# Kernel optimization log

Hardware: AMD Instinct MI355X
Metric: run time of the kernel (lower is better)

The kernel has to match this reference:

```python
import jax, jax.numpy as jnp
import numpy as np

NUM_HEADS = 16


def setup_inputs() -> dict:
    key = jax.random.key(0)
    k1, k2, k3 = jax.random.split(key, 3)
    T, B, E = 2048, 2, 1024
    query = jax.random.normal(k1, (T, B, E), dtype=jnp.float32)
    # xavier-uniform-ish init for qkv weight, small normal for output proj
    lim = (6.0 / (3 * E + E)) ** 0.5
    W_qkv = jax.random.uniform(k2, (3 * E, E), dtype=jnp.float32, minval=-lim, maxval=lim)
    W_o = jax.random.normal(k3, (E, E), dtype=jnp.float32) * 0.02
    b_qkv = jnp.zeros((3 * E,), dtype=jnp.float32)
    b_o = jnp.zeros((E,), dtype=jnp.float32)
    return {"query": query, "W_qkv": W_qkv, "b_qkv": b_qkv, "W_o": W_o, "b_o": b_o}


def reference(query, W_qkv, b_qkv, W_o, b_o):
    T, B, E = query.shape
    H = NUM_HEADS
    hd = E // H
    scaling = float(hd) ** -0.5

    # fused qkv projection: [T, B, 3E]
    qkv = jnp.einsum('tbe,fe->tbf', query, W_qkv) + b_qkv
    q, k, v = jnp.split(qkv, 3, axis=-1)
    q = q * scaling

    def to_heads(x):  # [T, B, E] -> [B*H, T, hd]
        return x.reshape(T, B * H, hd).transpose(1, 0, 2)

    q, k, v = to_heads(q), to_heads(k), to_heads(v)

    # explicit bmm QK^T -> softmax -> bmm AV (faithful to source)
    scores = jnp.einsum('bqd,bkd->bqk', q, k)          # [B*H, T, T]
    attn = jax.nn.softmax(scores, axis=-1)             # dropout p=0.0 (eval)
    ctx = jnp.einsum('bqk,bkd->bqd', attn, v)          # [B*H, T, hd]

    out = ctx.transpose(1, 0, 2).reshape(T, B, E)
    out = jnp.einsum('tbe,fe->tbf', out, W_o) + b_o    # o_net

    avg_weights = attn.reshape(B, H, T, T).sum(axis=1) / H  # need_weights=True path
    return out, avg_weights
```

## Files before the change

kernel.cpp:

```cpp
#include <hip/hip_runtime.h>
#include <stdint.h>

typedef unsigned short u16;
typedef __bf16 bf16x8 __attribute__((ext_vector_type(8)));
typedef float f32x4 __attribute__((ext_vector_type(4)));
typedef float f32x16 __attribute__((ext_vector_type(16)));

__device__ __forceinline__ u16 f2b(float f) {
  unsigned u = __builtin_bit_cast(unsigned, f);
  u += 0x7fffu + ((u >> 16) & 1u);
  return (u16)(u >> 16);
}

__device__ __forceinline__ float fexp2(float x) { return __builtin_amdgcn_exp2f(x); }

__device__ __forceinline__ void gld_lds16(const void* g, void* l) {
  __builtin_amdgcn_global_load_lds((const __attribute__((address_space(1))) unsigned int*)g,
                                   (__attribute__((address_space(3))) unsigned int*)l,
                                   16, 0, 0);
}

__global__ __launch_bounds__(256) void k_cvt(const float* __restrict__ s,
                                             u16* __restrict__ d, int n4) {
  int i = blockIdx.x * 256 + threadIdx.x;
  if (i >= n4) return;
  float4 v = reinterpret_cast<const float4*>(s)[i];
  ushort4 o;
  o.x = f2b(v.x); o.y = f2b(v.y); o.z = f2b(v.z); o.w = f2b(v.w);
  reinterpret_cast<ushort4*>(d)[i] = o;
}

template <int EPI>
__global__ __launch_bounds__(256) void k_gemm_nt(
    const u16* __restrict__ A, const u16* __restrict__ B, const float* __restrict__ bias,
    float* __restrict__ outF, u16* __restrict__ q_ws, u16* __restrict__ k_ws,
    u16* __restrict__ vt_ws) {
  __shared__ u16 Al[2][4096];
  __shared__ u16 Bl[2][4096];
  const int tid = threadIdx.x;
  const int w = tid >> 6, lane = tid & 63;
  const int wr = w >> 1, wc = w & 1;
  const int lo = lane & 15, hi = lane >> 4;
  const int tm = blockIdx.y, tn = blockIdx.x;
  const size_t arow0 = (size_t)tm * 128;
  const size_t brow0 = (size_t)tn * 128;

  f32x4 acc[4][4] = {};

  const int rr = lane >> 2;
  const int kc = (lane & 3) * 8;

  {
    const int k0 = kc;
    for (int rs = 0; rs < 2; ++rs) {
      int seg = rs * 4 + w;
      gld_lds16(A + (arow0 + seg * 16 + rr) * 1024 + k0, &Al[0][seg * 512 + lane * 8]);
      gld_lds16(B + (brow0 + seg * 16 + rr) * 1024 + k0, &Bl[0][seg * 512 + lane * 8]);
    }
  }
  __syncthreads();
  int cur = 0;
  for (int kb = 0; kb < 32; ++kb) {
    if (kb + 1 < 32) {
      const int k0 = (kb + 1) * 32 + kc;
      for (int rs = 0; rs < 2; ++rs) {
        int seg = rs * 4 + w;
        gld_lds16(A + (arow0 + seg * 16 + rr) * 1024 + k0, &Al[cur ^ 1][seg * 512 + lane * 8]);
        gld_lds16(B + (brow0 + seg * 16 + rr) * 1024 + k0, &Bl[cur ^ 1][seg * 512 + lane * 8]);
      }
    }
    bf16x8 af[4], bfr[4];
#pragma unroll
    for (int m = 0; m < 4; ++m)
      af[m] = *(const bf16x8*)&Al[cur][(wr * 64 + m * 16 + lo) * 32 + hi * 8];
#pragma unroll
    for (int n = 0; n < 4; ++n)
      bfr[n] = *(const bf16x8*)&Bl[cur][(wc * 64 + n * 16 + lo) * 32 + hi * 8];
#pragma unroll
    for (int m = 0; m < 4; ++m)
#pragma unroll
      for (int n = 0; n < 4; ++n)
        acc[m][n] = __builtin_amdgcn_mfma_f32_16x16x32_bf16(af[m], bfr[n], acc[m][n], 0, 0, 0);
    __syncthreads();
    cur ^= 1;
  }

  if (EPI == 0) {
#pragma unroll
    for (int n = 0; n < 4; ++n) {
      const int col = tn * 128 + wc * 64 + n * 16 + lo;
      const float bb = bias[col];
#pragma unroll
      for (int m = 0; m < 4; ++m)
#pragma unroll
        for (int r = 0; r < 4; ++r) {
          const int row = tm * 128 + wr * 64 + m * 16 + hi * 4 + r;
          outF[(size_t)row * 1024 + col] = acc[m][n][r] + bb;
        }
    }
  } else {
    const int sec = tn >> 3;
#pragma unroll
    for (int n = 0; n < 4; ++n) {
      const int cin = (tn & 7) * 128 + wc * 64 + n * 16 + lo;
      const int h = cin >> 6, d = cin & 63;
      const float bb = bias[sec * 1024 + cin];
#pragma unroll
      for (int m = 0; m < 4; ++m) {
        const int rowb = tm * 128 + wr * 64 + m * 16 + hi * 4;
        const int t0 = rowb >> 1;
        const float v0 = acc[m][n][0] + bb, v1 = acc[m][n][1] + bb;
        const float v2 = acc[m][n][2] + bb, v3 = acc[m][n][3] + bb;
        if (sec == 0) {
          const float s = 0.18033688f;
          q_ws[(((size_t)h * 2048 + t0) * 64) + d]            = f2b(v0 * s);
          q_ws[(((size_t)(16 + h) * 2048 + t0) * 64) + d]     = f2b(v1 * s);
          q_ws[(((size_t)h * 2048 + t0 + 1) * 64) + d]        = f2b(v2 * s);
          q_ws[(((size_t)(16 + h) * 2048 + t0 + 1) * 64) + d] = f2b(v3 * s);
        } else if (sec == 1) {
          k_ws[(((size_t)h * 2048 + t0) * 64) + d]            = f2b(v0);
          k_ws[(((size_t)(16 + h) * 2048 + t0) * 64) + d]     = f2b(v1);
          k_ws[(((size_t)h * 2048 + t0 + 1) * 64) + d]        = f2b(v2);
          k_ws[(((size_t)(16 + h) * 2048 + t0 + 1) * 64) + d] = f2b(v3);
        } else {
          const int tp0 = (t0 & ~12) | ((t0 & 4) << 1) | ((t0 & 8) >> 1);
          ushort2 p0, p1;
          p0.x = f2b(v0); p0.y = f2b(v2);
          p1.x = f2b(v1); p1.y = f2b(v3);
          *(ushort2*)(vt_ws + ((size_t)h * 64 + d) * 2048 + tp0) = p0;
          *(ushort2*)(vt_ws + ((size_t)(16 + h) * 64 + d) * 2048 + tp0) = p1;
        }
      }
    }
  }
}

__global__ __launch_bounds__(512) void k_flash(
    const u16* __restrict__ q_ws, const u16* __restrict__ k_ws, const u16* __restrict__ vt_ws,
    u16* __restrict__ ctx_ws, float* __restrict__ c_ws) {
  __shared__ __align__(16) u16 KVl[32768];
  const int tid = threadIdx.x, w = tid >> 6, lane = tid & 63;
  const int h = lane >> 5, l31 = lane & 31, l7 = lane & 7;
  const int hh = w >> 2;
  const int wq = w & 3;
  const int tid_h = tid & 255;

  const int flat = blockIdx.y * 16 + blockIdx.x;
  const int xcd = flat & 7, slot = flat >> 3;
  const int bh = xcd * 4 + (slot >> 4);
  const int qtile = slot & 15;
  const int b = bh >> 4, head = bh & 15;
  const int qbase = qtile * 128;
  const int qrow = qbase + wq * 32 + l31;

  bf16x8 qf[4];
#pragma unroll
  for (int j = 0; j < 4; ++j)
    qf[j] = *(const bf16x8*)(q_ws + ((size_t)bh * 2048 + qrow) * 64 + j * 16 + h * 8);

  const int srow = tid_h >> 3, schk = tid_h & 7;
  const int xc = (schk ^ (srow & 7)) * 8;
  const u16* kgA = k_ws + ((size_t)bh * 2048 + hh * 16 * 64 + srow) * 64 + xc;
  const u16* vgA = vt_ws + ((size_t)bh * 64 + srow) * 2048 + hh * 16 * 64 + xc;

  f32x16 ca0 = {}, ca1 = {};
  float lrow = 0.f;

  {
    u16* base = KVl + hh * 8192;
    gld_lds16(kgA,             base + tid_h * 8);
    gld_lds16(kgA + 32 * 64,   base + 2048 + tid_h * 8);
    gld_lds16(vgA,             base + 4096 + tid_h * 8);
    gld_lds16(vgA + 32 * 2048, base + 6144 + tid_h * 8);
  }
  __syncthreads();

  int cur = 0;
  for (int it = 0; it < 16; ++it) {
    if (it < 15) {
      u16* base = KVl + (cur ^ 1) * 16384 + hh * 8192;
      const u16* kgt = kgA + (size_t)(it + 1) * 4096;
      const u16* vgt = vgA + (it + 1) * 64;
      gld_lds16(kgt,             base + tid_h * 8);
      gld_lds16(kgt + 32 * 64,   base + 2048 + tid_h * 8);
      gld_lds16(vgt,             base + 4096 + tid_h * 8);
      gld_lds16(vgt + 32 * 2048, base + 6144 + tid_h * 8);
    }
    const char* Kb = (const char*)(KVl + cur * 16384 + hh * 8192);
    const char* Vb = Kb + 8192;

    f32x16 st0 = {}, st1 = {};
    __builtin_amdgcn_s_setprio(1);
#pragma unroll
    for (int j = 0; j < 4; ++j) {
      bf16x8 k0 = *(const bf16x8*)(Kb + l31 * 128 + (((2 * j + h) ^ l7) * 16));
      bf16x8 k1 = *(const bf16x8*)(Kb + (32 + l31) * 128 + (((2 * j + h) ^ l7) * 16));
      st0 = __builtin_amdgcn_mfma_f32_32x32x16_bf16(k0, qf[j], st0, 0, 0, 0);
      st1 = __builtin_amdgcn_mfma_f32_32x32x16_bf16(k1, qf[j], st1, 0, 0, 0);
    }
    __builtin_amdgcn_s_setprio(0);

    float ps0 = 0.f, ps1 = 0.f;
#pragma unroll
    for (int r = 0; r < 16; ++r) { float p = fexp2(st0[r]); st0[r] = p; ps0 += p; }
#pragma unroll
    for (int r = 0; r < 16; ++r) { float p = fexp2(st1[r]); st1[r] = p; ps1 += p; }
    float ps = ps0 + ps1;
    ps += __shfl_xor(ps, 32, 64);
    lrow += ps;

    bf16x8 pb00, pb01, pb10, pb11;
#pragma unroll
    for (int i = 0; i < 8; ++i) {
      pb00[i] = (__bf16)st0[i];
      pb01[i] = (__bf16)st0[8 + i];
      pb10[i] = (__bf16)st1[i];
      pb11[i] = (__bf16)st1[8 + i];
    }

    __builtin_amdgcn_s_setprio(1);
#pragma unroll
    for (int t2 = 0; t2 < 2; ++t2)
#pragma unroll
      for (int kp = 0; kp < 2; ++kp) {
        const int ch = (4 * t2 + 2 * kp + h) ^ l7;
        bf16x8 v0 = *(const bf16x8*)(Vb + l31 * 128 + ch * 16);
        bf16x8 v1 = *(const bf16x8*)(Vb + (32 + l31) * 128 + ch * 16);
        const bf16x8 pv = (t2 == 0) ? (kp == 0 ? pb00 : pb01) : (kp == 0 ? pb10 : pb11);
        ca0 = __builtin_amdgcn_mfma_f32_32x32x16_bf16(v0, pv, ca0, 0, 0, 0);
        ca1 = __builtin_amdgcn_mfma_f32_32x32x16_bf16(v1, pv, ca1, 0, 0, 0);
      }
    __builtin_amdgcn_s_setprio(0);

    __syncthreads();
    cur ^= 1;
  }

  float* F = (float*)KVl;
  if (w >= 4) {
    const int g = w - 4;
#pragma unroll
    for (int r = 0; r < 16; ++r) {
      F[g * 2048 + r * 64 + lane] = ca0[r];
      F[g * 2048 + (16 + r) * 64 + lane] = ca1[r];
    }
    F[8192 + g * 64 + lane] = lrow;
  }
  __syncthreads();
  u16* tw = (u16*)((char*)KVl + 34816 + w * 4096);
  if (w < 4) {
#pragma unroll
    for (int r = 0; r < 16; ++r) {
      ca0[r] += F[w * 2048 + r * 64 + lane];
      ca1[r] += F[w * 2048 + (16 + r) * 64 + lane];
    }
    lrow += F[8192 + w * 64 + lane];
    const float inv = 1.0f / lrow;
    if (lane < 32) c_ws[(size_t)bh * 2048 + qrow] = inv;
#pragma unroll
    for (int r = 0; r < 16; ++r) {
      const int d0 = (r & 3) + 8 * (r >> 2) + 4 * h;
      const int d1 = 32 + d0;
      *(u16*)((char*)tw + l31 * 128 + ((2 * d0) ^ (l7 << 4))) = f2b(ca0[r] * inv);
      *(u16*)((char*)tw + l31 * 128 + ((2 * d1) ^ (l7 << 4))) = f2b(ca1[r] * inv);
    }
  }
  __syncthreads();
  if (w < 4) {
#pragma unroll
    for (int it = 0; it < 4; ++it) {
      const int row = it * 8 + (lane >> 3);
      uint4 val = *(const uint4*)((const char*)tw + row * 128 + (((lane & 7) ^ (row & 7)) * 16));
      const int q = qbase + wq * 32 + row;
      *(uint4*)(ctx_ws + ((size_t)(q * 2 + b)) * 1024 + head * 64 + (lane & 7) * 8) = val;
    }
  }
}

__global__ __launch_bounds__(256) void k_avg(
    const u16* __restrict__ q_ws, const u16* __restrict__ k_ws,
    const float* __restrict__ c_ws, float* __restrict__ avg) {
  __shared__ __align__(16) u16 Kl[2][128 * 64];
  const int tid = threadIdx.x, w = tid >> 6, lane = tid & 63;
  const int lo = lane & 15, hi = lane >> 4;
  const int kbase = blockIdx.x * 128;
  const int qb = blockIdx.y * 64;
  const int b = blockIdx.z;
  const int qrow = qb + w * 16 + lo;
  const int qrow_base = qb + w * 16 + hi * 4;

  const int r0 = tid >> 3, c0 = tid & 7;
  const int ldsoff = r0 * 128 + ((c0 ^ (r0 & 7)) << 4);
  const u16* kg = k_ws + ((size_t)(b * 16) * 2048 + kbase + r0) * 64 + c0 * 8;
  const int l7 = lo & 7;

  float acc[8][4] = {};
  const f32x4 zero = {0.f, 0.f, 0.f, 0.f};

  uint4 rg0 = *(const uint4*)(kg);
  uint4 rg1 = *(const uint4*)(kg + 32 * 64);
  uint4 rg2 = *(const uint4*)(kg + 64 * 64);
  uint4 rg3 = *(const uint4*)(kg + 96 * 64);
  {
    char* dst = (char*)Kl[0] + ldsoff;
    *(uint4*)(dst) = rg0;
    *(uint4*)(dst + 32 * 128) = rg1;
    *(uint4*)(dst + 64 * 128) = rg2;
    *(uint4*)(dst + 96 * 128) = rg3;
  }
  __syncthreads();

  int cur = 0;
  for (int h = 0; h < 16; ++h) {
    const int bh = b * 16 + h;
    if (h + 1 < 16) {
      const u16* kgn = kg + (size_t)(h + 1) * 2048 * 64;
      rg0 = *(const uint4*)(kgn);
      rg1 = *(const uint4*)(kgn + 32 * 64);
      rg2 = *(const uint4*)(kgn + 64 * 64);
      rg3 = *(const uint4*)(kgn + 96 * 64);
    }
    const u16* qp = q_ws + ((size_t)bh * 2048 + qrow) * 64 + hi * 8;
    bf16x8 qf0 = *(const bf16x8*)qp;
    bf16x8 qf1 = *(const bf16x8*)(qp + 32);
    const float4 cf = *(const float4*)(c_ws + (size_t)bh * 2048 + qrow_base);
    const float cfa[4] = {cf.x, cf.y, cf.z, cf.w};
    const char* kbse = (const char*)Kl[cur];
#pragma unroll
    for (int n = 0; n < 8; ++n) {
      const char* kp = kbse + (n * 16 + lo) * 128;
      bf16x8 k0 = *(const bf16x8*)(kp + ((hi ^ l7) << 4));
      bf16x8 k1 = *(const bf16x8*)(kp + (((hi + 4) ^ l7) << 4));
      f32x4 s = __builtin_amdgcn_mfma_f32_16x16x32_bf16(qf0, k0, zero, 0, 0, 0);
      s = __builtin_amdgcn_mfma_f32_16x16x32_bf16(qf1, k1, s, 0, 0, 0);
#pragma unroll
      for (int r = 0; r < 4; ++r) acc[n][r] += fexp2(s[r]) * cfa[r];
    }
    if (h + 1 < 16) {
      char* dst = (char*)Kl[cur ^ 1] + ldsoff;
      *(uint4*)(dst) = rg0;
      *(uint4*)(dst + 32 * 128) = rg1;
      *(uint4*)(dst + 64 * 128) = rg2;
      *(uint4*)(dst + 96 * 128) = rg3;
      __syncthreads();
    }
    cur ^= 1;
  }

  const float s16 = 1.0f / 16.0f;
#pragma unroll
  for (int n = 0; n < 8; ++n)
#pragma unroll
    for (int r = 0; r < 4; ++r)
      avg[((size_t)(b * 2048 + qrow_base + r)) * 2048 + kbase + n * 16 + lo] = acc[n][r] * s16;
}

extern "C" void kernel_launch(void* const* d_in, const int* in_sizes, int n_in,
                              void* d_out, int out_size, void* d_ws, size_t ws_size,
                              hipStream_t stream) {
  const float* query = (const float*)d_in[0];
  const float* Wqkv  = (const float*)d_in[1];
  const float* bqkv  = (const float*)d_in[2];
  const float* Wo    = (const float*)d_in[3];
  const float* bo    = (const float*)d_in[4];
  float* out = (float*)d_out;
  float* avg = out + (size_t)4096 * 1024;

  char* ws = (char*)d_ws;
  u16* qbf    = (u16*)(ws);
  u16* ctx_ws = (u16*)(ws);
  u16*   wqkvbf = (u16*)(ws + 8388608);
  float* c_ws   = (float*)(ws + 8388608);
  u16* wobf  = (u16*)(ws + 14680064);
  u16* q_ws  = (u16*)(ws + 16777216);
  u16* k_ws  = (u16*)(ws + 25165824);
  u16* vt_ws = (u16*)(ws + 33554432);

  k_cvt<<<dim3(4096), dim3(256), 0, stream>>>(query, qbf, 1048576);
  k_cvt<<<dim3(3072), dim3(256), 0, stream>>>(Wqkv, wqkvbf, 786432);
  k_cvt<<<dim3(1024), dim3(256), 0, stream>>>(Wo, wobf, 262144);
  k_gemm_nt<1><<<dim3(24, 32), dim3(256), 0, stream>>>(
      qbf, wqkvbf, bqkv, nullptr, q_ws, k_ws, vt_ws);
  k_flash<<<dim3(16, 32), dim3(512), 0, stream>>>(
      q_ws, k_ws, vt_ws, ctx_ws, c_ws);
  k_avg<<<dim3(16, 32, 2), dim3(256), 0, stream>>>(
      q_ws, k_ws, c_ws, avg);
  k_gemm_nt<0><<<dim3(8, 32), dim3(256), 0, stream>>>(
      ctx_ws, wobf, bo, out, nullptr, nullptr, nullptr);
}
```

Baseline: 157.4 us.

## Double GEMM K-tile to 64 with XOR-swizzled LDS layout

The bf16 NT GEMM now stages 64-wide K tiles instead of 32-wide ones. That halves the number of main-loop iterations and barriers, with each tile feeding two MFMA sub-steps. The LDS layout uses an XOR swizzle of 16-byte chunks by row, so the fragment reads across lanes avoid bank conflicts. The barrier now sits at the top of each iteration, before the prefetch. This doubles the LDS footprint per block, which can reduce occupancy.

```diff
diff --git a/kernel.cpp b/kernel.cpp
--- a/kernel.cpp
+++ b/kernel.cpp
@@ -35,53 +35,61 @@
     const u16* __restrict__ A, const u16* __restrict__ B, const float* __restrict__ bias,
     float* __restrict__ outF, u16* __restrict__ q_ws, u16* __restrict__ k_ws,
     u16* __restrict__ vt_ws) {
-  __shared__ u16 Al[2][4096];
-  __shared__ u16 Bl[2][4096];
+  __shared__ __align__(16) u16 Al[2][8192];
+  __shared__ __align__(16) u16 Bl[2][8192];
   const int tid = threadIdx.x;
   const int w = tid >> 6, lane = tid & 63;
   const int wr = w >> 1, wc = w & 1;
   const int lo = lane & 15, hi = lane >> 4;
+  const int l7 = lane & 7;
   const int tm = blockIdx.y, tn = blockIdx.x;
   const size_t arow0 = (size_t)tm * 128;
   const size_t brow0 = (size_t)tn * 128;
 
   f32x4 acc[4][4] = {};
 
-  const int rr = lane >> 2;
-  const int kc = (lane & 3) * 8;
-
-  {
-    const int k0 = kc;
-    for (int rs = 0; rs < 2; ++rs) {
-      int seg = rs * 4 + w;
-      gld_lds16(A + (arow0 + seg * 16 + rr) * 1024 + k0, &Al[0][seg * 512 + lane * 8]);
-      gld_lds16(B + (brow0 + seg * 16 + rr) * 1024 + k0, &Bl[0][seg * 512 + lane * 8]);
-    }
-  }
-  __syncthreads();
+  const int rr0 = tid >> 3, cc = tid & 7;
+  const int xoff = (cc ^ (rr0 & 7)) * 8;
+  const u16* Asrc = A + (arow0 + rr0) * 1024 + xoff;
+  const u16* Bsrc = B + (brow0 + rr0) * 1024 + xoff;
+  const int ldst = rr0 * 64 + cc * 8;
+
+#pragma unroll
+  for (int j = 0; j < 4; ++j) {
+    gld_lds16(Asrc + j * 32 * 1024, &Al[0][ldst + j * 2048]);
+    gld_lds16(Bsrc + j * 32 * 1024, &Bl[0][ldst + j * 2048]);
+  }
+
   int cur = 0;
-  for (int kb = 0; kb < 32; ++kb) {
-    if (kb + 1 < 32) {
-      const int k0 = (kb + 1) * 32 + kc;
-      for (int rs = 0; rs < 2; ++rs) {
-        int seg = rs * 4 + w;
-        gld_lds16(A + (arow0 + seg * 16 + rr) * 1024 + k0, &Al[cur ^ 1][seg * 512 + lane * 8]);
-        gld_lds16(B + (brow0 + seg * 16 + rr) * 1024 + k0, &Bl[cur ^ 1][seg * 512 + lane * 8]);
-      }
-    }
-    bf16x8 af[4], bfr[4];
-#pragma unroll
-    for (int m = 0; m < 4; ++m)
-      af[m] = *(const bf16x8*)&Al[cur][(wr * 64 + m * 16 + lo) * 32 + hi * 8];
-#pragma unroll
-    for (int n = 0; n < 4; ++n)
-      bfr[n] = *(const bf16x8*)&Bl[cur][(wc * 64 + n * 16 + lo) * 32 + hi * 8];
-#pragma unroll
-    for (int m = 0; m < 4; ++m)
-#pragma unroll
-      for (int n = 0; n < 4; ++n)
-        acc[m][n] = __builtin_amdgcn_mfma_f32_16x16x32_bf16(af[m], bfr[n], acc[m][n], 0, 0, 0);
+  for (int kt = 0; kt < 16; ++kt) {
     __syncthreads();
+    if (kt < 15) {
+      const int koff = (kt + 1) * 64;
+#pragma unroll
+      for (int j = 0; j < 4; ++j) {
+        gld_lds16(Asrc + koff + j * 32 * 1024, &Al[cur ^ 1][ldst + j * 2048]);
+        gld_lds16(Bsrc + koff + j * 32 * 1024, &Bl[cur ^ 1][ldst + j * 2048]);
+      }
+    }
+#pragma unroll
+    for (int kh = 0; kh < 2; ++kh) {
+      bf16x8 af[4], bfr[4];
+#pragma unroll
+      for (int m = 0; m < 4; ++m) {
+        const int row = wr * 64 + m * 16 + lo;
+        af[m] = *(const bf16x8*)&Al[cur][row * 64 + (((kh * 4 + hi) ^ l7) * 8)];
+      }
+#pragma unroll
+      for (int n = 0; n < 4; ++n) {
+        const int row = wc * 64 + n * 16 + lo;
+        bfr[n] = *(const bf16x8*)&Bl[cur][row * 64 + (((kh * 4 + hi) ^ l7) * 8)];
+      }
+#pragma unroll
+      for (int m = 0; m < 4; ++m)
+#pragma unroll
+        for (int n = 0; n < 4; ++n)
+          acc[m][n] = __builtin_amdgcn_mfma_f32_16x16x32_bf16(af[m], bfr[n], acc[m][n], 0, 0, 0);
+    }
     cur ^= 1;
   }
 
```

Result: no change. 159.1 us (+1.1%).

## Merge conversion launches, swizzle GEMM LDS, and co-schedule output GEMM with avg kernel

Applied to the files above, without the earlier changes.

The three fp32->bf16 conversion launches become one kernel that picks its source by block index. The GEMM LDS layout gets an XOR swizzle on the k-chunk to cut bank conflicts on fragment reads. The output projection GEMM and the head-averaged attention-weight kernel, which are independent of each other, now run as one heterogeneous launch so their blocks can overlap and fill the GPU. This saves launch gaps and tail effects, but the combined kernel shares one LDS size and register budget between both bodies.

```diff
diff --git a/kernel.cpp b/kernel.cpp
--- a/kernel.cpp
+++ b/kernel.cpp
@@ -20,10 +20,18 @@
                                    16, 0, 0);
 }
 
-__global__ __launch_bounds__(256) void k_cvt(const float* __restrict__ s,
-                                             u16* __restrict__ d, int n4) {
-  int i = blockIdx.x * 256 + threadIdx.x;
-  if (i >= n4) return;
+__global__ __launch_bounds__(256) void k_cvt3(
+    const float* __restrict__ s0, u16* __restrict__ d0,
+    const float* __restrict__ s1, u16* __restrict__ d1,
+    const float* __restrict__ s2, u16* __restrict__ d2) {
+  const int bx = blockIdx.x;
+  const float* s;
+  u16* d;
+  int i0;
+  if (bx < 4096)      { s = s0; d = d0; i0 = bx; }
+  else if (bx < 7168) { s = s1; d = d1; i0 = bx - 4096; }
+  else                { s = s2; d = d2; i0 = bx - 7168; }
+  const int i = i0 * 256 + threadIdx.x;
   float4 v = reinterpret_cast<const float4*>(s)[i];
   ushort4 o;
   o.x = f2b(v.x); o.y = f2b(v.y); o.z = f2b(v.z); o.w = f2b(v.w);
@@ -31,51 +39,52 @@
 }
 
 template <int EPI>
-__global__ __launch_bounds__(256) void k_gemm_nt(
+__device__ __forceinline__ void gemm_body(
     const u16* __restrict__ A, const u16* __restrict__ B, const float* __restrict__ bias,
     float* __restrict__ outF, u16* __restrict__ q_ws, u16* __restrict__ k_ws,
-    u16* __restrict__ vt_ws) {
-  __shared__ u16 Al[2][4096];
-  __shared__ u16 Bl[2][4096];
+    u16* __restrict__ vt_ws, int tm, int tn, u16* smem) {
+  u16* Al0 = smem;
+  u16* Bl0 = smem + 8192;
   const int tid = threadIdx.x;
   const int w = tid >> 6, lane = tid & 63;
   const int wr = w >> 1, wc = w & 1;
   const int lo = lane & 15, hi = lane >> 4;
-  const int tm = blockIdx.y, tn = blockIdx.x;
   const size_t arow0 = (size_t)tm * 128;
   const size_t brow0 = (size_t)tn * 128;
 
   f32x4 acc[4][4] = {};
 
   const int rr = lane >> 2;
-  const int kc = (lane & 3) * 8;
-
-  {
-    const int k0 = kc;
-    for (int rs = 0; rs < 2; ++rs) {
-      int seg = rs * 4 + w;
-      gld_lds16(A + (arow0 + seg * 16 + rr) * 1024 + k0, &Al[0][seg * 512 + lane * 8]);
-      gld_lds16(B + (brow0 + seg * 16 + rr) * 1024 + k0, &Bl[0][seg * 512 + lane * 8]);
-    }
+  const int kswz = ((lane & 3) ^ ((rr >> 1) & 3)) * 8;
+  const int rsw = (lo >> 1) & 3;
+
+  for (int rs = 0; rs < 2; ++rs) {
+    int seg = rs * 4 + w;
+    gld_lds16(A + (arow0 + seg * 16 + rr) * 1024 + kswz, &Al0[seg * 512 + lane * 8]);
+    gld_lds16(B + (brow0 + seg * 16 + rr) * 1024 + kswz, &Bl0[seg * 512 + lane * 8]);
   }
   __syncthreads();
   int cur = 0;
   for (int kb = 0; kb < 32; ++kb) {
     if (kb + 1 < 32) {
-      const int k0 = (kb + 1) * 32 + kc;
+      const int k0 = (kb + 1) * 32 + kswz;
+      u16* Ad = Al0 + (cur ^ 1) * 4096;
+      u16* Bd = Bl0 + (cur ^ 1) * 4096;
       for (int rs = 0; rs < 2; ++rs) {
         int seg = rs * 4 + w;
-        gld_lds16(A + (arow0 + seg * 16 + rr) * 1024 + k0, &Al[cur ^ 1][seg * 512 + lane * 8]);
-        gld_lds16(B + (brow0 + seg * 16 + rr) * 1024 + k0, &Bl[cur ^ 1][seg * 512 + lane * 8]);
+        gld_lds16(A + (arow0 + seg * 16 + rr) * 1024 + k0, &Ad[seg * 512 + lane * 8]);
+        gld_lds16(B + (brow0 + seg * 16 + rr) * 1024 + k0, &Bd[seg * 512 + lane * 8]);
       }
     }
+    const u16* Ac = Al0 + cur * 4096;
+    const u16* Bc = Bl0 + cur * 4096;
     bf16x8 af[4], bfr[4];
 #pragma unroll
     for (int m = 0; m < 4; ++m)
-      af[m] = *(const bf16x8*)&Al[cur][(wr * 64 + m * 16 + lo) * 32 + hi * 8];
+      af[m] = *(const bf16x8*)&Ac[(wr * 64 + m * 16 + lo) * 32 + ((hi ^ rsw) * 8)];
 #pragma unroll
     for (int n = 0; n < 4; ++n)
-      bfr[n] = *(const bf16x8*)&Bl[cur][(wc * 64 + n * 16 + lo) * 32 + hi * 8];
+      bfr[n] = *(const bf16x8*)&Bc[(wc * 64 + n * 16 + lo) * 32 + ((hi ^ rsw) * 8)];
 #pragma unroll
     for (int m = 0; m < 4; ++m)
 #pragma unroll
@@ -135,6 +144,105 @@
   }
 }
 
+__global__ __launch_bounds__(256) void k_gemm_qkv(
+    const u16* __restrict__ A, const u16* __restrict__ B, const float* __restrict__ bias,
+    u16* __restrict__ q_ws, u16* __restrict__ k_ws, u16* __restrict__ vt_ws) {
+  __shared__ __align__(16) u16 smem[16384];
+  gemm_body<1>(A, B, bias, nullptr, q_ws, k_ws, vt_ws, blockIdx.y, blockIdx.x, smem);
+}
+
+__device__ __forceinline__ void avg_body(
+    const u16* __restrict__ q_ws, const u16* __restrict__ k_ws,
+    const float* __restrict__ c_ws, float* __restrict__ avg,
+    int kx, int qy, int b, u16* smem) {
+  u16* Kl0 = smem;
+  const int tid = threadIdx.x, w = tid >> 6, lane = tid & 63;
+  const int lo = lane & 15, hi = lane >> 4;
+  const int kbase = kx * 128;
+  const int qb = qy * 64;
+  const int qrow = qb + w * 16 + lo;
+  const int qrow_base = qb + w * 16 + hi * 4;
+
+  const int r0 = tid >> 3, c0 = tid & 7;
+  const int ldsoff = r0 * 128 + ((c0 ^ (r0 & 7)) << 4);
+  const u16* kg = k_ws + ((size_t)(b * 16) * 2048 + kbase + r0) * 64 + c0 * 8;
+  const int l7 = lo & 7;
+
+  float acc[8][4] = {};
+  const f32x4 zero = {0.f, 0.f, 0.f, 0.f};
+
+  uint4 rg0 = *(const uint4*)(kg);
+  uint4 rg1 = *(const uint4*)(kg + 32 * 64);
+  uint4 rg2 = *(const uint4*)(kg + 64 * 64);
+  uint4 rg3 = *(const uint4*)(kg + 96 * 64);
+  {
+    char* dst = (char*)Kl0 + ldsoff;
+    *(uint4*)(dst) = rg0;
+    *(uint4*)(dst + 32 * 128) = rg1;
+    *(uint4*)(dst + 64 * 128) = rg2;
+    *(uint4*)(dst + 96 * 128) = rg3;
+  }
+  __syncthreads();
+
+  int cur = 0;
+  for (int h = 0; h < 16; ++h) {
+    const int bh = b * 16 + h;
+    if (h + 1 < 16) {
+      const u16* kgn = kg + (size_t)(h + 1) * 2048 * 64;
+      rg0 = *(const uint4*)(kgn);
+      rg1 = *(const uint4*)(kgn + 32 * 64);
+      rg2 = *(const uint4*)(kgn + 64 * 64);
+      rg3 = *(const uint4*)(kgn + 96 * 64);
+    }
+    const u16* qp = q_ws + ((size_t)bh * 2048 + qrow) * 64 + hi * 8;
+    bf16x8 qf0 = *(const bf16x8*)qp;
+    bf16x8 qf1 = *(const bf16x8*)(qp + 32);
+    const float4 cf = *(const float4*)(c_ws + (size_t)bh * 2048 + qrow_base);
+    const float cfa[4] = {cf.x, cf.y, cf.z, cf.w};
+    const char* kbse = (const char*)(Kl0 + cur * 8192);
+#pragma unroll
+    for (int n = 0; n < 8; ++n) {
+      const char* kp = kbse + (n * 16 + lo) * 128;
+      bf16x8 k0 = *(const bf16x8*)(kp + ((hi ^ l7) << 4));
+      bf16x8 k1 = *(const bf16x8*)(kp + (((hi + 4) ^ l7) << 4));
+      f32x4 s = __builtin_amdgcn_mfma_f32_16x16x32_bf16(qf0, k0, zero, 0, 0, 0);
+      s = __builtin_amdgcn_mfma_f32_16x16x32_bf16(qf1, k1, s, 0, 0, 0);
+#pragma unroll
+      for (int r = 0; r < 4; ++r) acc[n][r] += fexp2(s[r]) * cfa[r];
+    }
+    if (h + 1 < 16) {
+      char* dst = (char*)(Kl0 + (cur ^ 1) * 8192) + ldsoff;
+      *(uint4*)(dst) = rg0;
+      *(uint4*)(dst + 32 * 128) = rg1;
+      *(uint4*)(dst + 64 * 128) = rg2;
+      *(uint4*)(dst + 96 * 128) = rg3;
+      __syncthreads();
+    }
+    cur ^= 1;
+  }
+
+  const float s16 = 1.0f / 16.0f;
+#pragma unroll
+  for (int n = 0; n < 8; ++n)
+#pragma unroll
+    for (int r = 0; r < 4; ++r)
+      avg[((size_t)(b * 2048 + qrow_base + r)) * 2048 + kbase + n * 16 + lo] = acc[n][r] * s16;
+}
+
+__global__ __launch_bounds__(256) void k_tail(
+    const u16* __restrict__ ctx, const u16* __restrict__ wobf, const float* __restrict__ bo,
+    float* __restrict__ out, const u16* __restrict__ q_ws, const u16* __restrict__ k_ws,
+    const float* __restrict__ c_ws, float* __restrict__ avg) {
+  __shared__ __align__(16) u16 smem[16384];
+  const int bx = blockIdx.x;
+  if (bx < 256) {
+    gemm_body<0>(ctx, wobf, bo, out, nullptr, nullptr, nullptr, bx >> 3, bx & 7, smem);
+  } else {
+    const int id = bx - 256;
+    avg_body(q_ws, k_ws, c_ws, avg, id & 15, (id >> 4) & 31, id >> 9, smem);
+  }
+}
+
 __global__ __launch_bounds__(512) void k_flash(
     const u16* __restrict__ q_ws, const u16* __restrict__ k_ws, const u16* __restrict__ vt_ws,
     u16* __restrict__ ctx_ws, float* __restrict__ c_ws) {
@@ -277,84 +385,6 @@
   }
 }
 
-__global__ __launch_bounds__(256) void k_avg(
-    const u16* __restrict__ q_ws, const u16* __restrict__ k_ws,
-    const float* __restrict__ c_ws, float* __restrict__ avg) {
-  __shared__ __align__(16) u16 Kl[2][128 * 64];
-  const int tid = threadIdx.x, w = tid >> 6, lane = tid & 63;
-  const int lo = lane & 15, hi = lane >> 4;
-  const int kbase = blockIdx.x * 128;
-  const int qb = blockIdx.y * 64;
-  const int b = blockIdx.z;
-  const int qrow = qb + w * 16 + lo;
-  const int qrow_base = qb + w * 16 + hi * 4;
-
-  const int r0 = tid >> 3, c0 = tid & 7;
-  const int ldsoff = r0 * 128 + ((c0 ^ (r0 & 7)) << 4);
-  const u16* kg = k_ws + ((size_t)(b * 16) * 2048 + kbase + r0) * 64 + c0 * 8;
-  const int l7 = lo & 7;
-
-  float acc[8][4] = {};
-  const f32x4 zero = {0.f, 0.f, 0.f, 0.f};
-
-  uint4 rg0 = *(const uint4*)(kg);
-  uint4 rg1 = *(const uint4*)(kg + 32 * 64);
-  uint4 rg2 = *(const uint4*)(kg + 64 * 64);
-  uint4 rg3 = *(const uint4*)(kg + 96 * 64);
-  {
-    char* dst = (char*)Kl[0] + ldsoff;
-    *(uint4*)(dst) = rg0;
-    *(uint4*)(dst + 32 * 128) = rg1;
-    *(uint4*)(dst + 64 * 128) = rg2;
-    *(uint4*)(dst + 96 * 128) = rg3;
-  }
-  __syncthreads();
-
-  int cur = 0;
-  for (int h = 0; h < 16; ++h) {
-    const int bh = b * 16 + h;
-    if (h + 1 < 16) {
-      const u16* kgn = kg + (size_t)(h + 1) * 2048 * 64;
-      rg0 = *(const uint4*)(kgn);
-      rg1 = *(const uint4*)(kgn + 32 * 64);
-      rg2 = *(const uint4*)(kgn + 64 * 64);
-      rg3 = *(const uint4*)(kgn + 96 * 64);
-    }
-    const u16* qp = q_ws + ((size_t)bh * 2048 + qrow) * 64 + hi * 8;
-    bf16x8 qf0 = *(const bf16x8*)qp;
-    bf16x8 qf1 = *(const bf16x8*)(qp + 32);
-    const float4 cf = *(const float4*)(c_ws + (size_t)bh * 2048 + qrow_base);
-    const float cfa[4] = {cf.x, cf.y, cf.z, cf.w};
-    const char* kbse = (const char*)Kl[cur];
-#pragma unroll
-    for (int n = 0; n < 8; ++n) {
-      const char* kp = kbse + (n * 16 + lo) * 128;
-      bf16x8 k0 = *(const bf16x8*)(kp + ((hi ^ l7) << 4));
-      bf16x8 k1 = *(const bf16x8*)(kp + (((hi + 4) ^ l7) << 4));
-      f32x4 s = __builtin_amdgcn_mfma_f32_16x16x32_bf16(qf0, k0, zero, 0, 0, 0);
-      s = __builtin_amdgcn_mfma_f32_16x16x32_bf16(qf1, k1, s, 0, 0, 0);
-#pragma unroll
-      for (int r = 0; r < 4; ++r) acc[n][r] += fexp2(s[r]) * cfa[r];
-    }
-    if (h + 1 < 16) {
-      char* dst = (char*)Kl[cur ^ 1] + ldsoff;
-      *(uint4*)(dst) = rg0;
-      *(uint4*)(dst + 32 * 128) = rg1;
-      *(uint4*)(dst + 64 * 128) = rg2;
-      *(uint4*)(dst + 96 * 128) = rg3;
-      __syncthreads();
-    }
-    cur ^= 1;
-  }
-
-  const float s16 = 1.0f / 16.0f;
-#pragma unroll
-  for (int n = 0; n < 8; ++n)
-#pragma unroll
-    for (int r = 0; r < 4; ++r)
-      avg[((size_t)(b * 2048 + qrow_base + r)) * 2048 + kbase + n * 16 + lo] = acc[n][r] * s16;
-}
-
 extern "C" void kernel_launch(void* const* d_in, const int* in_sizes, int n_in,
                               void* d_out, int out_size, void* d_ws, size_t ws_size,
                               hipStream_t stream) {
@@ -376,15 +406,11 @@
   u16* k_ws  = (u16*)(ws + 25165824);
   u16* vt_ws = (u16*)(ws + 33554432);
 
-  k_cvt<<<dim3(4096), dim3(256), 0, stream>>>(query, qbf, 1048576);
-  k_cvt<<<dim3(3072), dim3(256), 0, stream>>>(Wqkv, wqkvbf, 786432);
-  k_cvt<<<dim3(1024), dim3(256), 0, stream>>>(Wo, wobf, 262144);
-  k_gemm_nt<1><<<dim3(24, 32), dim3(256), 0, stream>>>(
-      qbf, wqkvbf, bqkv, nullptr, q_ws, k_ws, vt_ws);
+  k_cvt3<<<dim3(8192), dim3(256), 0, stream>>>(query, qbf, Wqkv, wqkvbf, Wo, wobf);
+  k_gemm_qkv<<<dim3(24, 32), dim3(256), 0, stream>>>(
+      qbf, wqkvbf, bqkv, q_ws, k_ws, vt_ws);
   k_flash<<<dim3(16, 32), dim3(512), 0, stream>>>(
       q_ws, k_ws, vt_ws, ctx_ws, c_ws);
-  k_avg<<<dim3(16, 32, 2), dim3(256), 0, stream>>>(
-      q_ws, k_ws, c_ws, avg);
-  k_gemm_nt<0><<<dim3(8, 32), dim3(256), 0, stream>>>(
-      ctx_ws, wobf, bo, out, nullptr, nullptr, nullptr);
-}
+  k_tail<<<dim3(1280), dim3(256), 0, stream>>>(
+      ctx_ws, wobf, bo, out, q_ws, k_ws, c_ws, avg);
+}
```

Result: faster. 141.3 us (-10.2%).
